# Optimization experiments

Measured on AMD Instinct MI355X. Metric: run time of the kernel, lower is better.

## Reference

```python
import jax, jax.numpy as jnp
import numpy as np
from jax import lax

NMS_TH = 0.05
TOPK_P = 1000
NMS_IOU = 0.5
NUMDETS = 100
NMS_ITERS = 15
IM = 2048.0
SIZES = [256, 128, 64, 32, 16]
NUM_CLASS = 80


def _make_boxes(key, n):
    k1, k2, k3, k4 = jax.random.split(key, 4)
    cy = jax.random.uniform(k1, (n,)) * IM
    cx = jax.random.uniform(k2, (n,)) * IM
    h = jax.random.uniform(k3, (n,)) * 300.0 + 16.0
    w = jax.random.uniform(k4, (n,)) * 300.0 + 16.0
    # yxyx boxes
    return jnp.stack([cy - h / 2, cx - w / 2, cy + h / 2, cx + w / 2], axis=1)


def setup_inputs() -> dict:
    key = jax.random.key(0)
    inp = {}
    for s, sz in enumerate(SIZES):
        kc = jax.random.fold_in(key, 2 * s)
        kb = jax.random.fold_in(key, 2 * s + 1)
        n = sz * sz
        inp['cls%d' % s] = jax.random.normal(kc, (1, n, NUM_CLASS), jnp.float32) - 2.0
        inp['reg%d' % s] = _make_boxes(kb, n)[None]
    inp['locations'] = jnp.array([0.0, 0.0, IM - 1.0, IM - 1.0, 1024.0, 1024.0], jnp.float32)
    return inp


def _pairwise_iou(a, b):
    # a: (N,4) yxyx, b: (M,4) yxyx -> (N,M)
    area_a = jnp.clip(a[:, 2] - a[:, 0], 0) * jnp.clip(a[:, 3] - a[:, 1], 0)
    area_b = jnp.clip(b[:, 2] - b[:, 0], 0) * jnp.clip(b[:, 3] - b[:, 1], 0)
    iy1 = jnp.maximum(a[:, None, 0], b[None, :, 0])
    ix1 = jnp.maximum(a[:, None, 1], b[None, :, 1])
    iy2 = jnp.minimum(a[:, None, 2], b[None, :, 2])
    ix2 = jnp.minimum(a[:, None, 3], b[None, :, 3])
    inter = jnp.clip(iy2 - iy1, 0) * jnp.clip(ix2 - ix1, 0)
    union = area_a[:, None] + area_b[None, :] - inter
    return inter / jnp.maximum(union, 1e-9)


def _cluster_nms(boxes, scores, classes, valid, iou_th):
    order = jnp.argsort(-scores)
    b = boxes[order]
    s = scores[order]
    c = classes[order]
    v = valid[order]
    iou = jnp.triu(_pairwise_iou(b, b), k=1)  # (K,K)

    def body(B, _):
        max_a = B.max(axis=0)
        keep_col = (max_a <= iou_th).astype(B.dtype)[:, None]
        return iou * keep_col, None

    B, _ = lax.scan(body, iou, None, length=NMS_ITERS)
    keep = (B.max(axis=0) <= iou_th) & v
    return b, s, c, keep


def _per_level(cls_s, reg_s):
    p = jax.nn.sigmoid(cls_s[0])                 # (N, C)
    ps = p.max(axis=1)                           # (N,)
    pi = p.argmax(axis=1).astype(jnp.int32) + 1  # class index, 0 is background
    m = ps > NMS_TH
    ps_m = jnp.where(m, ps, -1.0)
    k = min(TOPK_P, ps_m.shape[0])
    top_s, top_idx = lax.top_k(ps_m, k)
    return top_s, pi[top_idx], reg_s[0][top_idx], m[top_idx]


def reference(cls0, cls1, cls2, cls3, cls4, reg0, reg1, reg2, reg3, reg4, locations):
    levels = [(cls0, reg0), (cls1, reg1), (cls2, reg2), (cls3, reg3), (cls4, reg4)]
    sc, cl, bx, vd = [], [], [], []
    for cls_s, reg_s in levels:
        s_, c_, b_, v_ = _per_level(cls_s, reg_s)
        sc.append(s_); cl.append(c_); bx.append(b_); vd.append(v_)
    scores = jnp.concatenate(sc)
    classes = jnp.concatenate(cl)
    boxes = jnp.concatenate(bx, axis=0)
    valid = jnp.concatenate(vd)
    scores = jnp.where(valid, scores, 0.0)

    vy1, vx1, vy2, vx2 = locations[0], locations[1], locations[2], locations[3]
    ori_h, ori_w = locations[4], locations[5]
    boxes = jnp.stack([
        jnp.maximum(boxes[:, 0], vy1), jnp.maximum(boxes[:, 1], vx1),
        jnp.minimum(boxes[:, 2], vy2), jnp.minimum(boxes[:, 3], vx2)], axis=1)

    b, s, c, keep = _cluster_nms(boxes, scores, classes, valid, NMS_IOU)
    s = jnp.where(keep, s, 0.0)
    top_s, sel = lax.top_k(s, NUMDETS)
    bbox = b[sel]
    cls_out = c[sel]

    # transfer boxes back to original-image coordinates
    sy = ori_h / jnp.maximum(vy2 - vy1, 1e-6)
    sx = ori_w / jnp.maximum(vx2 - vx1, 1e-6)
    bbox = jnp.stack([
        (bbox[:, 0] - vy1) * sy, (bbox[:, 1] - vx1) * sx,
        (bbox[:, 2] - vy1) * sy, (bbox[:, 3] - vx1) * sx], axis=1)
    return bbox, cls_out, top_s
```

## Files before the change

kernel.cpp:

```cpp
#include <hip/hip_runtime.h>
#include <math.h>

#define NANCH 87296
#define NF 4256
#define CAPD 128
#define NBINS 65536
#define NITER 16
#define BCAP 2048
#define EC 8192
#define NBLK 341
#define BIN_NEG 0x407Fu

struct InPtrs {
    const float* cls[5];
    const float* reg[5];
    const float* loc;
};

constexpr size_t SZ_HIST  = 5ull * NBINS * 4;
constexpr size_t OFF_HIST = 0;
constexpr size_t OFF_CNT  = OFF_HIST + SZ_HIST;
constexpr size_t OFF_CTR  = OFF_CNT + (size_t)NF * 4;
constexpr size_t ZERO_SZ  = OFF_CTR + 64;
constexpr size_t OFF_SBITS = ((ZERO_SZ + 255) / 256) * 256;
constexpr size_t OFF_CLSV  = OFF_SBITS + (size_t)NANCH * 4;
constexpr size_t OFF_PAR   = OFF_CLSV + (size_t)NANCH * 4;
constexpr size_t OFF_INVB  = OFF_PAR + 128;
constexpr size_t OFF_INVO  = OFF_INVB + (size_t)NBLK * 4;
constexpr size_t OFF_FINK  = ((OFF_INVO + (size_t)NBLK * 4 + 255) / 256) * 256;
constexpr size_t OFF_BBUF  = OFF_FINK + (size_t)NF * 8;
constexpr size_t OFF_SBOX  = OFF_BBUF + 5ull * BCAP * 8;
constexpr size_t OFF_SSC   = OFF_SBOX + (size_t)NF * 16;
constexpr size_t OFF_SCV   = OFF_SSC + (size_t)NF * 4;
constexpr size_t OFF_SAR   = OFF_SCV + (size_t)NF * 4;
constexpr size_t OFF_NBR   = OFF_SAR + (size_t)NF * 4;

__device__ __forceinline__ void lvl_of(int a, int& lev, int& idx) {
    if (a < 65536)      { lev = 0; idx = a; }
    else if (a < 81920) { lev = 1; idx = a - 65536; }
    else if (a < 86016) { lev = 2; idx = a - 81920; }
    else if (a < 87040) { lev = 3; idx = a - 86016; }
    else                { lev = 4; idx = a - 87040; }
}

__device__ __forceinline__ unsigned int fkey(float f) {
    unsigned int u = __float_as_uint(f);
    return u ^ ((u & 0x80000000u) ? 0xFFFFFFFFu : 0x80000000u);
}
__device__ __forceinline__ float funkey(unsigned int k) {
    return __uint_as_float(k ^ ((k & 0x80000000u) ? 0x80000000u : 0xFFFFFFFFu));
}
__device__ __forceinline__ unsigned int binaddr(unsigned int bin) {
    return ((bin & 63u) << 10) | (bin >> 6);
}

__global__ __launch_bounds__(1024) void k1_score(InPtrs P, unsigned int* hist,
        unsigned int* sbits, unsigned int* clsv, unsigned int* invBlk) {
    int t = threadIdx.x;
    int a = blockIdx.x * 256 + (t >> 2);
    int k = t & 3;
    int lev, idx; lvl_of(a, lev, idx);
    const float4* row = (const float4*)(P.cls[lev] + (size_t)idx * 80);
    float best = -INFINITY; int bi = 0;
    #pragma unroll
    for (int q = 0; q < 5; ++q) {
        float4 v = row[q * 4 + k];
        int c0 = q * 16 + k * 4;
        if (v.x > best) { best = v.x; bi = c0 + 0; }
        if (v.y > best) { best = v.y; bi = c0 + 1; }
        if (v.z > best) { best = v.z; bi = c0 + 2; }
        if (v.w > best) { best = v.w; bi = c0 + 3; }
    }
    #pragma unroll
    for (int m = 1; m < 4; m <<= 1) {
        float ob = __shfl_xor(best, m, 64);
        int  obi = __shfl_xor(bi, m, 64);
        if (ob > best || (ob == best && obi < bi)) { best = ob; bi = obi; }
    }
    bool lead = (k == 0);
    unsigned int valid = 0;
    if (lead) {
        float score = 1.0f / (1.0f + expf(-best));
        valid = (score > 0.05f) ? 1u : 0u;
        float psm = valid ? score : -1.0f;
        unsigned int sb = fkey(psm);
        sbits[a] = sb;
        clsv[a] = (unsigned int)(bi + 1) | (valid << 31);
        if (valid) atomicAdd(&hist[(size_t)lev * NBINS + binaddr(sb >> 16)], 1u);
    }
    __shared__ unsigned int wv[16];
    unsigned long long mv = __ballot(lead && valid);
    int lane = t & 63, w = t >> 6;
    if (lane == 0) wv[w] = (unsigned int)__popcll(mv);
    __syncthreads();
    if (t == 0) {
        unsigned int s = 0;
        #pragma unroll
        for (int i = 0; i < 16; ++i) s += wv[i];
        invBlk[blockIdx.x] = 256u - s;
    }
}

__global__ __launch_bounds__(1024) void k2_scan(const unsigned int* hist,
        const unsigned int* invBlk, unsigned int* params, unsigned int* invOff) {
    int t = threadIdx.x;
    if (blockIdx.x == 5) {
        __shared__ unsigned int sv[512];
        __shared__ unsigned int orig[512];
        if (t < 512) {
            unsigned int v = (t < NBLK) ? invBlk[t] : 0u;
            sv[t] = v; orig[t] = v;
        }
        __syncthreads();
        for (int off = 1; off < 512; off <<= 1) {
            unsigned int add = 0;
            if (t < 512 && t >= off) add = sv[t - off];
            __syncthreads();
            if (t < 512) sv[t] += add;
            __syncthreads();
        }
        if (t < NBLK) {
            int segStart = (t < 256) ? 0 : (t < 320) ? 256 : (t < 336) ? 320
                         : (t < 340) ? 336 : 340;
            invOff[t] = sv[t] - orig[t] - (segStart > 0 ? sv[segStart - 1] : 0u);
        }
        return;
    }
    int lev = blockIdx.x;
    unsigned int K = (lev == 4) ? 256u : 1000u;
    const unsigned int* h = hist + (size_t)lev * NBINS;
    __shared__ unsigned int seg[1024];
    __shared__ unsigned int suf[1024];
    unsigned int s = 0;
    #pragma unroll 8
    for (int q = 0; q < 64; ++q) s += h[(q << 10) | t];
    seg[t] = s;
    suf[t] = s;
    __syncthreads();
    for (int off = 1; off < 1024; off <<= 1) {
        unsigned int v = suf[t];
        unsigned int add = (t + off < 1024) ? suf[t + off] : 0u;
        __syncthreads();
        suf[t] = v + add;
        __syncthreads();
    }
    unsigned int totValid = suf[0];
    if (totValid >= K) {
        unsigned int excl = suf[t] - seg[t];
        if (excl < K && excl + seg[t] >= K) {
            unsigned int cum = excl;
            for (int b = 63; b >= 0; --b) {
                unsigned int c = h[(b << 10) | t];
                if (cum + c >= K) {
                    params[lev] = (unsigned int)(t * 64 + b);
                    params[8 + lev] = K - cum;
                    params[16 + lev] = 0;
                    break;
                }
                cum += c;
            }
        }
    } else if (t == 0) {
        params[lev] = BIN_NEG;
        params[8 + lev] = 0;
        params[16 + lev] = K - totValid;
    }
}

__global__ __launch_bounds__(256) void k3_compact(const unsigned int* sbits,
        const unsigned int* clsv, const unsigned int* params,
        const unsigned int* invOff, unsigned long long* finKeys,
        unsigned int* ctrs, unsigned long long* bBuf) {
    int blk = blockIdx.x;
    int t = threadIdx.x;
    int a = blk * 256 + t;
    int lev, idx; lvl_of(a, lev, idx);
    unsigned int sb = sbits[a];
    unsigned int cv = clsv[a];
    unsigned int h16 = sb >> 16;
    unsigned int Bs = params[lev];
    unsigned int rNeg = params[16 + lev];
    unsigned int valid = cv >> 31;
    int lane = t & 63, w = t >> 6;
    unsigned long long lt = (1ull << lane) - 1ull;
    __shared__ unsigned int wInv[4], wFin[4], wB[4];
    __shared__ unsigned int baseFin, baseB;
    unsigned long long mInv = __ballot(valid == 0u);
    if (lane == 0) wInv[w] = (unsigned int)__popcll(mInv);
    __syncthreads();
    unsigned int invRank = invOff[blk] + (unsigned int)__popcll(mInv & lt);
    for (int i = 0; i < w; ++i) invRank += wInv[i];
    bool isFin, isB;
    if (valid) {
        isFin = (h16 > Bs);
        isB   = (h16 == Bs);
    } else {
        isFin = (Bs == BIN_NEG) && (invRank < rNeg);
        isB   = false;
    }
    unsigned long long mFin = __ballot(isFin);
    unsigned long long mB   = __ballot(isB);
    if (lane == 0) { wFin[w] = (unsigned int)__popcll(mFin); wB[w] = (unsigned int)__popcll(mB); }
    __syncthreads();
    if (t == 0) {
        unsigned int tf = wFin[0] + wFin[1] + wFin[2] + wFin[3];
        unsigned int tb = wB[0] + wB[1] + wB[2] + wB[3];
        baseFin = tf ? atomicAdd(&ctrs[0], tf) : 0u;
        baseB   = tb ? atomicAdd(&ctrs[1 + lev], tb) : 0u;
    }
    __syncthreads();
    if (isFin || isB) {
        unsigned int composite = ((unsigned int)lev << 16) | (unsigned int)idx;
        unsigned int inv = (~composite) & 0x7FFFFu;
        unsigned int low = (inv << 13) | (valid << 7) | (cv & 0x7Fu);
        unsigned long long key = ((unsigned long long)sb << 32) | low;
        if (isFin) {
            unsigned int p = baseFin + (unsigned int)__popcll(mFin & lt);
            for (int i = 0; i < w; ++i) p += wFin[i];
            if (p < NF) finKeys[p] = key;
        } else {
            unsigned int p = baseB + (unsigned int)__popcll(mB & lt);
            for (int i = 0; i < w; ++i) p += wB[i];
            if (p < BCAP) bBuf[(size_t)lev * BCAP + p] = key;
        }
    }
}

__global__ __launch_bounds__(256) void k5_rank(InPtrs P,
        const unsigned long long* finKeys, const unsigned int* ctrs,
        const unsigned int* params, const unsigned long long* bBuf,
        float4* sBox, float* sScore, unsigned int* sCV, float* sArea) {
    __shared__ unsigned long long keys[NF];
    __shared__ unsigned long long kb[BCAP];
    __shared__ unsigned int rnk[64];
    int t = threadIdx.x;
    unsigned int fc = ctrs[0];
    if (fc > NF) fc = NF;
    for (int i = t; i < (int)fc; i += 256) keys[i] = finKeys[i];
    if (t < 64) rnk[t] = 0;
    __syncthreads();
    unsigned int pos = fc;
    for (int lev = 0; lev < 5; ++lev) {
        unsigned int bc = ctrs[1 + lev];
        int n = (bc > BCAP) ? BCAP : (int)bc;
        int r = (int)params[8 + lev];
        if (r > n) r = n;
        if (r > 0) {
            int m = 1; while (m < n) m <<= 1;
            for (int i = t; i < m; i += 256)
                kb[i] = (i < n) ? bBuf[(size_t)lev * BCAP + i] : 0ull;
            __syncthreads();
            for (int len = 2; len <= m; len <<= 1) {
                for (int st = len >> 1; st > 0; st >>= 1) {
                    for (int i = t; i < m; i += 256) {
                        int j = i ^ st;
                        if (j > i) {
                            unsigned long long a = kb[i], b = kb[j];
                            bool up = ((i & len) == 0);
                            if (up ? (a < b) : (a > b)) { kb[i] = b; kb[j] = a; }
                        }
                    }
                    __syncthreads();
                }
            }
            for (int i = t; i < r; i += 256)
                if (pos + (unsigned int)i < NF) keys[pos + i] = kb[i];
            pos += (unsigned int)r;
            __syncthreads();
        }
    }
    for (int i = (int)pos + t; i < NF; i += 256) keys[i] = (unsigned long long)i;
    __syncthreads();
    int lf = t & 63;
    int seg = t >> 6;
    int f = blockIdx.x * 64 + lf;
    unsigned long long my = (f < NF) ? keys[f] : 0ull;
    if (f < NF) {
        unsigned int c = 0;
        int s0 = seg * 1064, s1 = s0 + 1064;
        for (int i = s0; i < s1; ++i) c += (keys[i] > my) ? 1u : 0u;
        atomicAdd(&rnk[lf], c);
    }
    __syncthreads();
    if (seg == 0 && f < NF) {
        unsigned int r = rnk[lf];
        unsigned int sb  = (unsigned int)(my >> 32);
        unsigned int low = (unsigned int)my;
        unsigned int composite = (~(low >> 13)) & 0x7FFFFu;
        int lev = composite >> 16;
        int idx = composite & 0xFFFF;
        float4 b = ((const float4*)P.reg[lev])[idx];
        float vy1 = P.loc[0], vx1 = P.loc[1], vy2 = P.loc[2], vx2 = P.loc[3];
        float y1 = fmaxf(b.x, vy1), x1 = fmaxf(b.y, vx1);
        float y2 = fminf(b.z, vy2), x2 = fminf(b.w, vx2);
        float area = __fmul_rn(fmaxf(y2 - y1, 0.0f), fmaxf(x2 - x1, 0.0f));
        unsigned int valid = (low >> 7) & 1u;
        sBox[r] = make_float4(y1, x1, y2, x2);
        sScore[r] = valid ? funkey(sb) : 0.0f;
        sCV[r] = (low & 0x7Fu) | (valid << 31);
        sArea[r] = area;
    }
}

__global__ __launch_bounds__(256) void k6_adj(const float4* sBox,
        const float* sArea, unsigned int* cnt, unsigned short* nbr) {
    int L = blockIdx.x;
    float fr = sqrtf(8.0f * (float)L + 1.0f);
    int jt = (int)((fr - 1.0f) * 0.5f);
    while ((jt + 1) * (jt + 2) / 2 <= L) jt++;
    while (jt * (jt + 1) / 2 > L) jt--;
    int it = L - jt * (jt + 1) / 2;
    __shared__ float4 cb[64]; __shared__ float ca[64];
    __shared__ float4 rb[64]; __shared__ float ra[64];
    int t = threadIdx.x;
    if (t < 64) {
        int j = jt * 64 + t;
        if (j < NF) { cb[t] = sBox[j]; ca[t] = sArea[j]; }
        int i = it * 64 + t;
        if (i < NF) { rb[t] = sBox[i]; ra[t] = sArea[i]; }
    }
    __syncthreads();
    int lj = t & 63;
    int j = jt * 64 + lj;
    if (j >= NF) return;
    float4 B = cb[lj]; float ab = ca[lj];
    for (int li = (t >> 6); li < 64; li += 4) {
        int i = it * 64 + li;
        if (i >= j) continue;
        float4 A = rb[li]; float aa = ra[li];
        float iy1 = fmaxf(A.x, B.x), ix1 = fmaxf(A.y, B.y);
        float iy2 = fminf(A.z, B.z), ix2 = fminf(A.w, B.w);
        float ih = fmaxf(iy2 - iy1, 0.0f), iw = fmaxf(ix2 - ix1, 0.0f);
        float inter = __fmul_rn(ih, iw);
        float uni = __fsub_rn(__fadd_rn(aa, ab), inter);
        float iou = __fdiv_rn(inter, fmaxf(uni, 1e-9f));
        if (iou > 0.5f) {
            unsigned int p = atomicAdd(&cnt[j], 1u);
            if (p < CAPD) nbr[(size_t)j * CAPD + p] = (unsigned short)i;
        }
    }
}

__global__ __launch_bounds__(1024) void k7_nms(InPtrs P, const float4* sBox,
        const float* sScore, const unsigned int* sCV, const unsigned int* cnt,
        const unsigned short* nbr, float* out) {
    __shared__ unsigned int off[NF + 1];
    __shared__ unsigned int edges[EC];
    __shared__ __align__(4) unsigned char bufA[NF];
    __shared__ __align__(4) unsigned char bufB[NF];
    __shared__ unsigned int csum[1024];
    __shared__ float ploc[6];
    int t = threadIdx.x;
    if (t < 6) ploc[t] = P.loc[t];
    const int CH = 5;
    unsigned int dq[CH];
    {
        unsigned int s = 0;
        #pragma unroll
        for (int q = 0; q < CH; ++q) {
            int j = t * CH + q;
            unsigned int d = 0;
            if (j < NF) { d = cnt[j]; if (d > CAPD) d = CAPD; }
            dq[q] = d; s += d;
        }
        csum[t] = s;
        for (int j = t; j < NF; j += 1024) bufA[j] = 1;
        __syncthreads();
        for (int o = 1; o < 1024; o <<= 1) {
            unsigned int v = csum[t];
            unsigned int add = (t >= o) ? csum[t - o] : 0u;
            __syncthreads();
            csum[t] = v + add;
            __syncthreads();
        }
        unsigned int base = csum[t] - s;
        #pragma unroll
        for (int q = 0; q < CH; ++q) {
            int j = t * CH + q;
            if (j < NF) { off[j] = base; base += dq[q]; }
        }
        if (t == 1023) off[NF] = csum[1023];
    }
    __syncthreads();
    unsigned int E = off[NF];
    bool useLds = (E <= (unsigned int)EC);
    if (useLds) {
        #pragma unroll
        for (int q = 0; q < CH; ++q) {
            int j = t * CH + q;
            if (j < NF) {
                unsigned int o = off[j];
                unsigned int d = dq[q];
                const unsigned short* nl = nbr + (size_t)j * CAPD;
                for (unsigned int e = 0; e < d; ++e)
                    edges[o + e] = ((unsigned int)nl[e] << 16) | (unsigned int)j;
            }
        }
    }
    __syncthreads();
    unsigned char* cur = bufA; unsigned char* nxt = bufB;
    if (useLds) {
        for (int itr = 0; itr < NITER; ++itr) {
            if (t < (NF + 3) / 4) ((unsigned int*)nxt)[t] = 0x01010101u;
            __syncthreads();
            for (int e = t; e < (int)E; e += 1024) {
                unsigned int pk = edges[e];
                if (cur[pk >> 16]) nxt[pk & 0xFFFFu] = 0;
            }
            __syncthreads();
            unsigned char* tm = cur; cur = nxt; nxt = tm;
        }
    } else {
        for (int itr = 0; itr < NITER; ++itr) {
            for (int j = t; j < NF; j += 1024) {
                unsigned int d = cnt[j]; if (d > CAPD) d = CAPD;
                const unsigned short* nl = nbr + (size_t)j * CAPD;
                unsigned char kp = 1;
                for (unsigned int e = 0; e < d; ++e)
                    if (cur[nl[e]]) { kp = 0; break; }
                nxt[j] = kp;
            }
            __syncthreads();
            unsigned char* tm = cur; cur = nxt; nxt = tm;
        }
    }
    int base = t * CH;
    unsigned char kf[CH];
    unsigned int sum = 0;
    #pragma unroll
    for (int q = 0; q < CH; ++q) {
        int j = base + q;
        unsigned char v = 0;
        if (j < NF) v = cur[j] & (unsigned char)(sCV[j] >> 31);
        kf[q] = v; sum += v;
    }
    csum[t] = sum;
    __syncthreads();
    for (int o = 1; o < 1024; o <<= 1) {
        unsigned int v = csum[t];
        unsigned int add = (t >= o) ? csum[t - o] : 0u;
        __syncthreads();
        csum[t] = v + add;
        __syncthreads();
    }
    unsigned int keptTot = csum[1023];
    unsigned int run = csum[t] - sum;
    float vy1 = ploc[0], vx1 = ploc[1], vy2 = ploc[2], vx2 = ploc[3];
    float sy = ploc[4] / fmaxf(vy2 - vy1, 1e-6f);
    float sx = ploc[5] / fmaxf(vx2 - vx1, 1e-6f);
    #pragma unroll
    for (int q = 0; q < CH; ++q) {
        int j = base + q;
        if (j >= NF) break;
        unsigned int slot = 0xFFFFFFFFu;
        float sc = 0.0f;
        if (kf[q]) {
            if (run < 100u) { slot = run; sc = sScore[j]; }
            run++;
        } else if (keptTot < 100u) {
            unsigned int nk = (unsigned int)j - run;
            unsigned int s2 = keptTot + nk;
            if (s2 < 100u) { slot = s2; sc = 0.0f; }
        }
        if (slot < 100u) {
            float4 b = sBox[j];
            out[slot * 4 + 0] = (b.x - vy1) * sy;
            out[slot * 4 + 1] = (b.y - vx1) * sx;
            out[slot * 4 + 2] = (b.z - vy1) * sy;
            out[slot * 4 + 3] = (b.w - vx1) * sx;
            out[400 + slot] = (float)(sCV[j] & 0x7Fu);
            out[500 + slot] = sc;
        }
    }
}

extern "C" void kernel_launch(void* const* d_in, const int* in_sizes, int n_in,
                              void* d_out, int out_size, void* d_ws, size_t ws_size,
                              hipStream_t stream) {
    (void)n_in; (void)out_size; (void)ws_size;
    InPtrs P;
    bool inter = (in_sizes[1] == 65536 * 4);
    for (int s = 0; s < 5; ++s) {
        P.cls[s] = (const float*)d_in[inter ? 2 * s : s];
        P.reg[s] = (const float*)d_in[inter ? 2 * s + 1 : 5 + s];
    }
    P.loc = (const float*)d_in[10];

    char* w = (char*)d_ws;
    unsigned int* hist   = (unsigned int*)(w + OFF_HIST);
    unsigned int* cnt    = (unsigned int*)(w + OFF_CNT);
    unsigned int* ctrs   = (unsigned int*)(w + OFF_CTR);
    unsigned int* sbits  = (unsigned int*)(w + OFF_SBITS);
    unsigned int* clsv   = (unsigned int*)(w + OFF_CLSV);
    unsigned int* params = (unsigned int*)(w + OFF_PAR);
    unsigned int* invBlk = (unsigned int*)(w + OFF_INVB);
    unsigned int* invOff = (unsigned int*)(w + OFF_INVO);
    unsigned long long* finKeys = (unsigned long long*)(w + OFF_FINK);
    unsigned long long* bBuf    = (unsigned long long*)(w + OFF_BBUF);
    float4* sBox  = (float4*)(w + OFF_SBOX);
    float* sScore = (float*)(w + OFF_SSC);
    unsigned int* sCV = (unsigned int*)(w + OFF_SCV);
    float* sArea  = (float*)(w + OFF_SAR);
    unsigned short* nbr = (unsigned short*)(w + OFF_NBR);

    hipMemsetAsync(d_ws, 0, ZERO_SZ, stream);
    k1_score<<<NBLK, 1024, 0, stream>>>(P, hist, sbits, clsv, invBlk);
    k2_scan<<<6, 1024, 0, stream>>>(hist, invBlk, params, invOff);
    k3_compact<<<NBLK, 256, 0, stream>>>(sbits, clsv, params, invOff, finKeys, ctrs, bBuf);
    k5_rank<<<67, 256, 0, stream>>>(P, finKeys, ctrs, params, bBuf, sBox, sScore, sCV, sArea);
    k6_adj<<<2278, 256, 0, stream>>>(sBox, sArea, cnt, nbr);
    k7_nms<<<1, 1024, 0, stream>>>(P, sBox, sScore, sCV, cnt, nbr, (float*)d_out);
}
```

Baseline: 196.9 us.

## Replace per-level bitonic sort with rank-count selection and vectorize rank loop

```diff
diff --git a/kernel.cpp b/kernel.cpp
--- a/kernel.cpp
+++ b/kernel.cpp
@@ -230,55 +230,54 @@
         const unsigned long long* finKeys, const unsigned int* ctrs,
         const unsigned int* params, const unsigned long long* bBuf,
         float4* sBox, float* sScore, unsigned int* sCV, float* sArea) {
-    __shared__ unsigned long long keys[NF];
-    __shared__ unsigned long long kb[BCAP];
+    __shared__ __align__(16) unsigned long long keys[NF];
+    __shared__ __align__(16) unsigned long long kb[BCAP];
     __shared__ unsigned int rnk[64];
+    __shared__ unsigned int posS;
     int t = threadIdx.x;
     unsigned int fc = ctrs[0];
     if (fc > NF) fc = NF;
     for (int i = t; i < (int)fc; i += 256) keys[i] = finKeys[i];
     if (t < 64) rnk[t] = 0;
-    __syncthreads();
-    unsigned int pos = fc;
+    if (t == 0) posS = fc;
+    __syncthreads();
     for (int lev = 0; lev < 5; ++lev) {
         unsigned int bc = ctrs[1 + lev];
         int n = (bc > BCAP) ? BCAP : (int)bc;
         int r = (int)params[8 + lev];
         if (r > n) r = n;
         if (r > 0) {
-            int m = 1; while (m < n) m <<= 1;
-            for (int i = t; i < m; i += 256)
-                kb[i] = (i < n) ? bBuf[(size_t)lev * BCAP + i] : 0ull;
-            __syncthreads();
-            for (int len = 2; len <= m; len <<= 1) {
-                for (int st = len >> 1; st > 0; st >>= 1) {
-                    for (int i = t; i < m; i += 256) {
-                        int j = i ^ st;
-                        if (j > i) {
-                            unsigned long long a = kb[i], b = kb[j];
-                            bool up = ((i & len) == 0);
-                            if (up ? (a < b) : (a > b)) { kb[i] = b; kb[j] = a; }
-                        }
-                    }
-                    __syncthreads();
+            for (int i = t; i < n; i += 256) kb[i] = bBuf[(size_t)lev * BCAP + i];
+            __syncthreads();
+            for (int i = t; i < n; i += 256) {
+                unsigned long long my = kb[i];
+                unsigned int c = 0;
+                #pragma unroll 4
+                for (int j = 0; j < n; ++j) c += (kb[j] > my) ? 1u : 0u;
+                if (c < (unsigned int)r) {
+                    unsigned int p = atomicAdd(&posS, 1u);
+                    if (p < NF) keys[p] = my;
                 }
             }
-            for (int i = t; i < r; i += 256)
-                if (pos + (unsigned int)i < NF) keys[pos + i] = kb[i];
-            pos += (unsigned int)r;
-            __syncthreads();
-        }
-    }
+            __syncthreads();
+        }
+    }
+    unsigned int pos = posS;
     for (int i = (int)pos + t; i < NF; i += 256) keys[i] = (unsigned long long)i;
     __syncthreads();
     int lf = t & 63;
     int seg = t >> 6;
     int f = blockIdx.x * 64 + lf;
-    unsigned long long my = (f < NF) ? keys[f] : 0ull;
-    if (f < NF) {
+    unsigned long long my = (f < NF) ? keys[f] : ~0ull;
+    {
         unsigned int c = 0;
-        int s0 = seg * 1064, s1 = s0 + 1064;
-        for (int i = s0; i < s1; ++i) c += (keys[i] > my) ? 1u : 0u;
+        const ulonglong2* kp = (const ulonglong2*)keys + seg * 532;
+        #pragma unroll 4
+        for (int i = 0; i < 532; ++i) {
+            ulonglong2 v = kp[i];
+            c += (v.x > my) ? 1u : 0u;
+            c += (v.y > my) ? 1u : 0u;
+        }
         atomicAdd(&rnk[lf], c);
     }
     __syncthreads();
```

Result: faster. 187.7 us (-4.7%).
